# Performance work log

Measured on AMD Instinct MI355X. Metric: run time of the kernel, lower is better.

Reference implementation:

```python
import jax, jax.numpy as jnp
import numpy as np

B, D, DEPTH, C = 8192, 2048, 10, 1000
NUM_INNER = 2 ** DEPTH - 1   # 1023
NUM_LEAVES = 2 ** DEPTH      # 1024


def setup_inputs() -> dict:
    key = jax.random.key(0)
    k1, k2, k3, k4 = jax.random.split(key, 4)
    x = jax.random.normal(k1, (B, D), dtype=jnp.float32)
    # scale weights like a typical init so sigmoid isn't fully saturated
    W = jax.random.normal(k2, (D, NUM_INNER), dtype=jnp.float32) * 0.02
    b = jax.random.normal(k3, (NUM_INNER,), dtype=jnp.float32) * 0.02
    leaf_dist = jax.random.normal(k4, (NUM_LEAVES, C), dtype=jnp.float32)
    return {"x": x, "W": W, "b": b, "leaf_dist": leaf_dist}


def reference(x, W, b, leaf_dist):
    # inner node routing probabilities: [B, num_inner]
    decisions = jax.nn.sigmoid(x @ W + b)
    depth = int(np.log2(decisions.shape[1] + 1))
    pp = jnp.ones((x.shape[0], 1), dtype=x.dtype)  # path probs, starts at root
    for d in range(depth):  # small fixed loop over tree depth
        s, e = 2 ** d - 1, 2 ** (d + 1) - 1
        ld = decisions[:, s:e]                      # [B, 2^d]
        pp = jnp.concatenate([pp * ld, pp * (1.0 - ld)], axis=1)  # [B, 2^(d+1)]
        # faithful reproduction of the original's even/odd reordering
        pp = jnp.concatenate([pp[:, ::2], pp[:, 1::2]], axis=1)
    leaf_probs = jax.nn.softmax(leaf_dist, axis=1)  # [num_leaves, C]
    return pp @ leaf_probs                          # [B, C]
```

## Files before the change

kernel.cpp:

```cpp
#include <hip/hip_runtime.h>

typedef __attribute__((ext_vector_type(8))) unsigned short ushort8v;
typedef __attribute__((ext_vector_type(8))) __bf16 bf16x8;
typedef __attribute__((ext_vector_type(4))) float floatx4;

__device__ __forceinline__ unsigned short f2b(float f) {
    unsigned u = __float_as_uint(f);
    unsigned r = u + 0x7fffu + ((u >> 16) & 1u);
    return (unsigned short)(r >> 16);
}
__device__ __forceinline__ float b2f(unsigned short h) {
    return __uint_as_float(((unsigned)h) << 16);
}

__device__ __forceinline__ void async_cp16(const void* g, void* l) {
    __builtin_amdgcn_global_load_lds(
        (__attribute__((address_space(1))) void*)g,
        (__attribute__((address_space(3))) void*)l,
        16, 0, 0);
}

__global__ __launch_bounds__(256) void cvt_f32_bf16(const float* __restrict__ in,
                                                    unsigned short* __restrict__ out,
                                                    int n4) {
    int i = blockIdx.x * 256 + threadIdx.x;
    if (i < n4) {
        float4 v = ((const float4*)in)[i];
        ushort4 o;
        o.x = f2b(v.x); o.y = f2b(v.y); o.z = f2b(v.z); o.w = f2b(v.w);
        ((ushort4*)out)[i] = o;
    }
}

__global__ __launch_bounds__(256) void transpose_W(const float* __restrict__ W,
                                                   unsigned short* __restrict__ Wt) {
    __shared__ float tile[32][33];
    int tx = threadIdx.x, ty = threadIdx.y;
    int n0 = blockIdx.x * 32, k0 = blockIdx.y * 32;
#pragma unroll
    for (int i = 0; i < 4; i++) {
        int k = k0 + ty + i * 8, n = n0 + tx;
        tile[ty + i * 8][tx] = (n < 1023) ? W[(size_t)k * 1023 + n] : 0.f;
    }
    __syncthreads();
#pragma unroll
    for (int i = 0; i < 4; i++) {
        int n = n0 + ty + i * 8, k = k0 + tx;
        Wt[(size_t)n * 2048 + k] = f2b(tile[tx][ty + i * 8]);
    }
}

__global__ __launch_bounds__(256) void softmax_rows(const float* __restrict__ ld_,
                                                    unsigned short* __restrict__ P) {
    __shared__ float buf[1000];
    __shared__ float red[8];
    int t = threadIdx.x;
    const float* r = ld_ + (size_t)blockIdx.x * 1000;
    float mx = -3.4e38f;
    for (int i = t; i < 1000; i += 256) { float v = r[i]; buf[i] = v; mx = fmaxf(mx, v); }
#pragma unroll
    for (int o = 32; o > 0; o >>= 1) mx = fmaxf(mx, __shfl_down(mx, o));
    if ((t & 63) == 0) red[t >> 6] = mx;
    __syncthreads();
    mx = fmaxf(fmaxf(red[0], red[1]), fmaxf(red[2], red[3]));
    float s = 0.f;
    for (int i = t; i < 1000; i += 256) { float e = __expf(buf[i] - mx); buf[i] = e; s += e; }
#pragma unroll
    for (int o = 32; o > 0; o >>= 1) s += __shfl_down(s, o);
    if ((t & 63) == 0) red[4 + (t >> 6)] = s;
    __syncthreads();
    float inv = 1.f / (red[4] + red[5] + red[6] + red[7]);
    unsigned short* out = P + (size_t)blockIdx.x * 1000;
    for (int i = t; i < 1000; i += 256) out[i] = f2b(buf[i] * inv);
}

__global__ __launch_bounds__(256) void transpose_P(const unsigned short* __restrict__ P,
                                                   unsigned short* __restrict__ Pt) {
    __shared__ unsigned short tile[32][33];
    int tx = threadIdx.x, ty = threadIdx.y;
    int c0 = blockIdx.x * 32, l0 = blockIdx.y * 32;
#pragma unroll
    for (int i = 0; i < 4; i++) {
        int c = c0 + tx, l = l0 + ty + i * 8;
        tile[ty + i * 8][tx] = (c < 1000) ? P[(size_t)l * 1000 + c] : (unsigned short)0;
    }
    __syncthreads();
#pragma unroll
    for (int i = 0; i < 4; i++) {
        Pt[(size_t)(c0 + ty + i * 8) * 1024 + l0 + tx] = tile[tx][ty + i * 8];
    }
}

__global__ __launch_bounds__(256) void pp_kernel(unsigned short* __restrict__ dec) {
    __shared__ float d[1024];
    __shared__ float pa[1024], pb[1024];
    const int t = threadIdx.x;
    unsigned short* row = dec + (size_t)blockIdx.x * 1024;
    for (int i = t; i < 1024; i += 256) d[i] = (i < 1023) ? b2f(row[i]) : 0.f;
    if (t == 0) pa[0] = 1.f;
    __syncthreads();
    float* cur = pa; float* nxt = pb;
    for (int dep = 0; dep < 10; dep++) {
        const int half = 1 << dep;
        const int len = half << 1;
        for (int j = t; j < len; j += 256) {
            int tt = j >> dep;
            int s  = j & (half - 1);
            int i2 = 2 * s + tt;
            int u  = i2 >> dep;
            int rr = i2 & (half - 1);
            float dv = d[half - 1 + rr];
            nxt[j] = cur[rr] * (u ? (1.f - dv) : dv);
        }
        __syncthreads();
        float* tmp = cur; cur = nxt; nxt = tmp;
    }
    for (int i = t; i < 1024; i += 256) row[i] = f2b(cur[i]);
}

#define BM 128
#define BN 128
#define BK 32

template <int EPI>
__global__ __launch_bounds__(256) void gemm_bt(const unsigned short* __restrict__ A,
                                               const unsigned short* __restrict__ Bt,
                                               const float* __restrict__ bias,
                                               unsigned short* __restrict__ obf,
                                               float* __restrict__ of32,
                                               int K, int ldo) {
    __shared__ __align__(16) unsigned short As[BM * BK];
    __shared__ __align__(16) unsigned short Bs[BN * BK];
    const int tid  = threadIdx.x;
    const int lane = tid & 63;
    const int wave = tid >> 6;
    const int wr = wave >> 1, wc = wave & 1;
    const int quad = lane >> 4, l16 = lane & 15;

    const int l   = blockIdx.x;
    const int xcd = l & 7;
    const int j   = l >> 3;
    const int bm  = (xcd * 8 + (j & 7)) * BM;
    const int bn  = (j >> 3) * BN;

    const int srow = tid >> 2;
    const int lg   = (tid & 3) ^ ((srow >> 1) & 3);
    const int scol = lg * 8;

    const unsigned short* Ag = A + (size_t)(bm + srow) * K + scol;
    const unsigned short* Bg = Bt + (size_t)(bn + srow) * K + scol;
    unsigned short* AsW = As + wave * 512;
    unsigned short* BsW = Bs + wave * 512;

    const int pgA = (quad ^ ((l16 >> 1) & 3)) * 8;

    floatx4 acc[4][4] = {};

    for (int k0 = 0; k0 < K; k0 += BK) {
        async_cp16(Ag + k0, AsW);
        async_cp16(Ag + (size_t)64 * K + k0, AsW + 2048);
        async_cp16(Bg + k0, BsW);
        async_cp16(Bg + (size_t)64 * K + k0, BsW + 2048);
        __syncthreads();

        bf16x8 af[4], bfr[4];
#pragma unroll
        for (int mi = 0; mi < 4; mi++)
            af[mi] = __builtin_bit_cast(bf16x8,
                *(const ushort8v*)(As + (wr * 64 + mi * 16 + l16) * BK + pgA));
#pragma unroll
        for (int ni = 0; ni < 4; ni++)
            bfr[ni] = __builtin_bit_cast(bf16x8,
                *(const ushort8v*)(Bs + (wc * 64 + ni * 16 + l16) * BK + pgA));
#pragma unroll
        for (int mi = 0; mi < 4; mi++)
#pragma unroll
            for (int ni = 0; ni < 4; ni++)
                acc[mi][ni] = __builtin_amdgcn_mfma_f32_16x16x32_bf16(
                    af[mi], bfr[ni], acc[mi][ni], 0, 0, 0);
        __syncthreads();
    }

#pragma unroll
    for (int ni = 0; ni < 4; ni++) {
        const int col = bn + wc * 64 + ni * 16 + l16;
        float bb = 0.f;
        if constexpr (EPI == 0) bb = (col < 1023) ? bias[col] : 0.f;
#pragma unroll
        for (int mi = 0; mi < 4; mi++) {
            const int row0 = bm + wr * 64 + mi * 16 + quad * 4;
#pragma unroll
            for (int r = 0; r < 4; r++) {
                float v = acc[mi][ni][r];
                if constexpr (EPI == 0) {
                    float sgm = 1.f / (1.f + __expf(-(v + bb)));
                    obf[(size_t)(row0 + r) * ldo + col] = f2b(sgm);
                } else {
                    if (col < 1000) of32[(size_t)(row0 + r) * ldo + col] = v;
                }
            }
        }
    }
}

extern "C" void kernel_launch(void* const* d_in, const int* in_sizes, int n_in,
                              void* d_out, int out_size, void* d_ws, size_t ws_size,
                              hipStream_t stream) {
    const float* x   = (const float*)d_in[0];
    const float* W   = (const float*)d_in[1];
    const float* b   = (const float*)d_in[2];
    const float* ldd = (const float*)d_in[3];
    float* out = (float*)d_out;

    char* ws = (char*)d_ws;
    unsigned short* xb  = (unsigned short*)(ws);
    unsigned short* Wt  = (unsigned short*)(ws + 33554432);
    unsigned short* dec = (unsigned short*)(ws + 37748736);
    unsigned short* P   = (unsigned short*)(ws + 54525952);
    unsigned short* Pt  = (unsigned short*)(ws + 56574208);

    cvt_f32_bf16<<<16384, 256, 0, stream>>>(x, xb, 4194304);
    transpose_W<<<dim3(32, 64), dim3(32, 8), 0, stream>>>(W, Wt);
    softmax_rows<<<1024, 256, 0, stream>>>(ldd, P);
    transpose_P<<<dim3(32, 32), dim3(32, 8), 0, stream>>>(P, Pt);

    gemm_bt<0><<<512, 256, 0, stream>>>(xb, Wt, b, dec, nullptr, 2048, 1024);
    pp_kernel<<<8192, 256, 0, stream>>>(dec);
    gemm_bt<1><<<512, 256, 0, stream>>>(dec, Pt, nullptr, nullptr, out, 1024, 1000);
}
```

Before: 227.9 us.

## Merge prep kernels into combined launches and halve GEMM tile rows

Folds the x conversion, W transpose and leaf softmax into one launch, and the P transpose into the path-probability kernel, cutting seven launches to four. The GEMM tile shrinks from 128x128 to 64x128 with a doubled grid and a launch-bounds occupancy hint, which gives more blocks per CU on a 256-CU part. Smaller tiles lower operand reuse per block. The fused kernels' shared memory is sized for the largest branch, which can lower occupancy for the light blocks.

```diff
diff --git a/kernel.cpp b/kernel.cpp
--- a/kernel.cpp
+++ b/kernel.cpp
@@ -20,128 +20,130 @@
         16, 0, 0);
 }
 
-__global__ __launch_bounds__(256) void cvt_f32_bf16(const float* __restrict__ in,
-                                                    unsigned short* __restrict__ out,
-                                                    int n4) {
-    int i = blockIdx.x * 256 + threadIdx.x;
-    if (i < n4) {
-        float4 v = ((const float4*)in)[i];
+__global__ __launch_bounds__(256) void prep_kernel(const float* __restrict__ x,
+                                                   unsigned short* __restrict__ xb,
+                                                   const float* __restrict__ W,
+                                                   unsigned short* __restrict__ Wt,
+                                                   const float* __restrict__ ld_,
+                                                   unsigned short* __restrict__ P) {
+    __shared__ float tile[32 * 33];
+    __shared__ float buf[1000];
+    __shared__ float red[8];
+    const int b = blockIdx.x, t = threadIdx.x;
+    if (b < 16384) {
+        int i = b * 256 + t;
+        float4 v = ((const float4*)x)[i];
         ushort4 o;
         o.x = f2b(v.x); o.y = f2b(v.y); o.z = f2b(v.z); o.w = f2b(v.w);
-        ((ushort4*)out)[i] = o;
-    }
-}
-
-__global__ __launch_bounds__(256) void transpose_W(const float* __restrict__ W,
-                                                   unsigned short* __restrict__ Wt) {
-    __shared__ float tile[32][33];
-    int tx = threadIdx.x, ty = threadIdx.y;
-    int n0 = blockIdx.x * 32, k0 = blockIdx.y * 32;
-#pragma unroll
-    for (int i = 0; i < 4; i++) {
-        int k = k0 + ty + i * 8, n = n0 + tx;
-        tile[ty + i * 8][tx] = (n < 1023) ? W[(size_t)k * 1023 + n] : 0.f;
-    }
-    __syncthreads();
-#pragma unroll
-    for (int i = 0; i < 4; i++) {
-        int n = n0 + ty + i * 8, k = k0 + tx;
-        Wt[(size_t)n * 2048 + k] = f2b(tile[tx][ty + i * 8]);
-    }
-}
-
-__global__ __launch_bounds__(256) void softmax_rows(const float* __restrict__ ld_,
-                                                    unsigned short* __restrict__ P) {
-    __shared__ float buf[1000];
-    __shared__ float red[8];
-    int t = threadIdx.x;
-    const float* r = ld_ + (size_t)blockIdx.x * 1000;
-    float mx = -3.4e38f;
-    for (int i = t; i < 1000; i += 256) { float v = r[i]; buf[i] = v; mx = fmaxf(mx, v); }
-#pragma unroll
-    for (int o = 32; o > 0; o >>= 1) mx = fmaxf(mx, __shfl_down(mx, o));
-    if ((t & 63) == 0) red[t >> 6] = mx;
-    __syncthreads();
-    mx = fmaxf(fmaxf(red[0], red[1]), fmaxf(red[2], red[3]));
-    float s = 0.f;
-    for (int i = t; i < 1000; i += 256) { float e = __expf(buf[i] - mx); buf[i] = e; s += e; }
-#pragma unroll
-    for (int o = 32; o > 0; o >>= 1) s += __shfl_down(s, o);
-    if ((t & 63) == 0) red[4 + (t >> 6)] = s;
-    __syncthreads();
-    float inv = 1.f / (red[4] + red[5] + red[6] + red[7]);
-    unsigned short* out = P + (size_t)blockIdx.x * 1000;
-    for (int i = t; i < 1000; i += 256) out[i] = f2b(buf[i] * inv);
-}
-
-__global__ __launch_bounds__(256) void transpose_P(const unsigned short* __restrict__ P,
-                                                   unsigned short* __restrict__ Pt) {
-    __shared__ unsigned short tile[32][33];
-    int tx = threadIdx.x, ty = threadIdx.y;
-    int c0 = blockIdx.x * 32, l0 = blockIdx.y * 32;
-#pragma unroll
-    for (int i = 0; i < 4; i++) {
-        int c = c0 + tx, l = l0 + ty + i * 8;
-        tile[ty + i * 8][tx] = (c < 1000) ? P[(size_t)l * 1000 + c] : (unsigned short)0;
-    }
-    __syncthreads();
-#pragma unroll
-    for (int i = 0; i < 4; i++) {
-        Pt[(size_t)(c0 + ty + i * 8) * 1024 + l0 + tx] = tile[tx][ty + i * 8];
-    }
-}
-
-__global__ __launch_bounds__(256) void pp_kernel(unsigned short* __restrict__ dec) {
-    __shared__ float d[1024];
-    __shared__ float pa[1024], pb[1024];
-    const int t = threadIdx.x;
-    unsigned short* row = dec + (size_t)blockIdx.x * 1024;
-    for (int i = t; i < 1024; i += 256) d[i] = (i < 1023) ? b2f(row[i]) : 0.f;
-    if (t == 0) pa[0] = 1.f;
-    __syncthreads();
-    float* cur = pa; float* nxt = pb;
-    for (int dep = 0; dep < 10; dep++) {
-        const int half = 1 << dep;
-        const int len = half << 1;
-        for (int j = t; j < len; j += 256) {
-            int tt = j >> dep;
-            int s  = j & (half - 1);
-            int i2 = 2 * s + tt;
-            int u  = i2 >> dep;
-            int rr = i2 & (half - 1);
-            float dv = d[half - 1 + rr];
-            nxt[j] = cur[rr] * (u ? (1.f - dv) : dv);
-        }
-        __syncthreads();
-        float* tmp = cur; cur = nxt; nxt = tmp;
-    }
-    for (int i = t; i < 1024; i += 256) row[i] = f2b(cur[i]);
-}
-
-#define BM 128
+        ((ushort4*)xb)[i] = o;
+    } else if (b < 16384 + 2048) {
+        int idx = b - 16384;
+        int n0 = (idx & 31) * 32, k0 = (idx >> 5) * 32;
+        int tx = t & 31, ty = t >> 5;
+#pragma unroll
+        for (int i = 0; i < 4; i++) {
+            int k = k0 + ty + i * 8, n = n0 + tx;
+            tile[(ty + i * 8) * 33 + tx] = (n < 1023) ? W[(size_t)k * 1023 + n] : 0.f;
+        }
+        __syncthreads();
+#pragma unroll
+        for (int i = 0; i < 4; i++) {
+            int n = n0 + ty + i * 8, k = k0 + tx;
+            Wt[(size_t)n * 2048 + k] = f2b(tile[tx * 33 + ty + i * 8]);
+        }
+    } else {
+        int row = b - 18432;
+        const float* r = ld_ + (size_t)row * 1000;
+        float mx = -3.4e38f;
+        for (int i = t; i < 1000; i += 256) { float v = r[i]; buf[i] = v; mx = fmaxf(mx, v); }
+#pragma unroll
+        for (int o = 32; o > 0; o >>= 1) mx = fmaxf(mx, __shfl_down(mx, o));
+        if ((t & 63) == 0) red[t >> 6] = mx;
+        __syncthreads();
+        mx = fmaxf(fmaxf(red[0], red[1]), fmaxf(red[2], red[3]));
+        float s = 0.f;
+        for (int i = t; i < 1000; i += 256) { float e = __expf(buf[i] - mx); buf[i] = e; s += e; }
+#pragma unroll
+        for (int o = 32; o > 0; o >>= 1) s += __shfl_down(s, o);
+        if ((t & 63) == 0) red[4 + (t >> 6)] = s;
+        __syncthreads();
+        float inv = 1.f / (red[4] + red[5] + red[6] + red[7]);
+        unsigned short* out = P + (size_t)row * 1000;
+        for (int i = t; i < 1000; i += 256) out[i] = f2b(buf[i] * inv);
+    }
+}
+
+__global__ __launch_bounds__(256) void pp_transP_kernel(unsigned short* __restrict__ dec,
+                                                        const unsigned short* __restrict__ P,
+                                                        unsigned short* __restrict__ Pt) {
+    __shared__ float smem[3072];
+    const int b = blockIdx.x, t = threadIdx.x;
+    if (b < 8192) {
+        float* d = smem; float* pa = smem + 1024; float* pb = smem + 2048;
+        unsigned short* row = dec + (size_t)b * 1024;
+        for (int i = t; i < 1024; i += 256) d[i] = (i < 1023) ? b2f(row[i]) : 0.f;
+        if (t == 0) pa[0] = 1.f;
+        __syncthreads();
+        float* cur = pa; float* nxt = pb;
+        for (int dep = 0; dep < 10; dep++) {
+            const int half = 1 << dep;
+            const int len = half << 1;
+            for (int j = t; j < len; j += 256) {
+                int tt = j >> dep;
+                int s  = j & (half - 1);
+                int i2 = 2 * s + tt;
+                int u  = i2 >> dep;
+                int rr = i2 & (half - 1);
+                float dv = d[half - 1 + rr];
+                nxt[j] = cur[rr] * (u ? (1.f - dv) : dv);
+            }
+            __syncthreads();
+            float* tmp = cur; cur = nxt; nxt = tmp;
+        }
+        for (int i = t; i < 1024; i += 256) row[i] = f2b(cur[i]);
+    } else {
+        int idx = b - 8192;
+        int c0 = (idx & 31) * 32, l0 = (idx >> 5) * 32;
+        int tx = t & 31, ty = t >> 5;
+        unsigned short* tile = (unsigned short*)smem;
+#pragma unroll
+        for (int i = 0; i < 4; i++) {
+            int c = c0 + tx, l = l0 + ty + i * 8;
+            tile[(ty + i * 8) * 33 + tx] = (c < 1000) ? P[(size_t)l * 1000 + c] : (unsigned short)0;
+        }
+        __syncthreads();
+#pragma unroll
+        for (int i = 0; i < 4; i++) {
+            Pt[(size_t)(c0 + ty + i * 8) * 1024 + l0 + tx] = tile[tx * 33 + ty + i * 8];
+        }
+    }
+}
+
+#define BM 64
 #define BN 128
 #define BK 32
 
 template <int EPI>
-__global__ __launch_bounds__(256) void gemm_bt(const unsigned short* __restrict__ A,
-                                               const unsigned short* __restrict__ Bt,
-                                               const float* __restrict__ bias,
-                                               unsigned short* __restrict__ obf,
-                                               float* __restrict__ of32,
-                                               int K, int ldo) {
+__global__ __launch_bounds__(256, 4) void gemm_bt(const unsigned short* __restrict__ A,
+                                                  const unsigned short* __restrict__ Bt,
+                                                  const float* __restrict__ bias,
+                                                  unsigned short* __restrict__ obf,
+                                                  float* __restrict__ of32,
+                                                  int K, int ldo) {
     __shared__ __align__(16) unsigned short As[BM * BK];
     __shared__ __align__(16) unsigned short Bs[BN * BK];
     const int tid  = threadIdx.x;
     const int lane = tid & 63;
     const int wave = tid >> 6;
-    const int wr = wave >> 1, wc = wave & 1;
+    const int wrow = (wave >> 1) * 32;
+    const int wcol = (wave & 1) * 64;
     const int quad = lane >> 4, l16 = lane & 15;
 
     const int l   = blockIdx.x;
     const int xcd = l & 7;
     const int j   = l >> 3;
-    const int bm  = (xcd * 8 + (j & 7)) * BM;
-    const int bn  = (j >> 3) * BN;
+    const int bm  = (xcd * 16 + (j & 15)) * BM;
+    const int bn  = (j >> 4) * BN;
 
     const int srow = tid >> 2;
     const int lg   = (tid & 3) ^ ((srow >> 1) & 3);
@@ -152,28 +154,27 @@
     unsigned short* AsW = As + wave * 512;
     unsigned short* BsW = Bs + wave * 512;
 
-    const int pgA = (quad ^ ((l16 >> 1) & 3)) * 8;
-
-    floatx4 acc[4][4] = {};
+    const int pg = (quad ^ ((l16 >> 1) & 3)) * 8;
+
+    floatx4 acc[2][4] = {};
 
     for (int k0 = 0; k0 < K; k0 += BK) {
         async_cp16(Ag + k0, AsW);
-        async_cp16(Ag + (size_t)64 * K + k0, AsW + 2048);
         async_cp16(Bg + k0, BsW);
         async_cp16(Bg + (size_t)64 * K + k0, BsW + 2048);
         __syncthreads();
 
-        bf16x8 af[4], bfr[4];
-#pragma unroll
-        for (int mi = 0; mi < 4; mi++)
+        bf16x8 af[2], bfr[4];
+#pragma unroll
+        for (int mi = 0; mi < 2; mi++)
             af[mi] = __builtin_bit_cast(bf16x8,
-                *(const ushort8v*)(As + (wr * 64 + mi * 16 + l16) * BK + pgA));
+                *(const ushort8v*)(As + (wrow + mi * 16 + l16) * BK + pg));
 #pragma unroll
         for (int ni = 0; ni < 4; ni++)
             bfr[ni] = __builtin_bit_cast(bf16x8,
-                *(const ushort8v*)(Bs + (wc * 64 + ni * 16 + l16) * BK + pgA));
-#pragma unroll
-        for (int mi = 0; mi < 4; mi++)
+                *(const ushort8v*)(Bs + (wcol + ni * 16 + l16) * BK + pg));
+#pragma unroll
+        for (int mi = 0; mi < 2; mi++)
 #pragma unroll
             for (int ni = 0; ni < 4; ni++)
                 acc[mi][ni] = __builtin_amdgcn_mfma_f32_16x16x32_bf16(
@@ -183,12 +184,12 @@
 
 #pragma unroll
     for (int ni = 0; ni < 4; ni++) {
-        const int col = bn + wc * 64 + ni * 16 + l16;
+        const int col = bn + wcol + ni * 16 + l16;
         float bb = 0.f;
         if constexpr (EPI == 0) bb = (col < 1023) ? bias[col] : 0.f;
 #pragma unroll
-        for (int mi = 0; mi < 4; mi++) {
-            const int row0 = bm + wr * 64 + mi * 16 + quad * 4;
+        for (int mi = 0; mi < 2; mi++) {
+            const int row0 = bm + wrow + mi * 16 + quad * 4;
 #pragma unroll
             for (int r = 0; r < 4; r++) {
                 float v = acc[mi][ni][r];
@@ -219,12 +220,8 @@
     unsigned short* P   = (unsigned short*)(ws + 54525952);
     unsigned short* Pt  = (unsigned short*)(ws + 56574208);
 
-    cvt_f32_bf16<<<16384, 256, 0, stream>>>(x, xb, 4194304);
-    transpose_W<<<dim3(32, 64), dim3(32, 8), 0, stream>>>(W, Wt);
-    softmax_rows<<<1024, 256, 0, stream>>>(ldd, P);
-    transpose_P<<<dim3(32, 32), dim3(32, 8), 0, stream>>>(P, Pt);
-
-    gemm_bt<0><<<512, 256, 0, stream>>>(xb, Wt, b, dec, nullptr, 2048, 1024);
-    pp_kernel<<<8192, 256, 0, stream>>>(dec);
-    gemm_bt<1><<<512, 256, 0, stream>>>(dec, Pt, nullptr, nullptr, out, 1024, 1000);
-}
+    prep_kernel<<<16384 + 2048 + 1024, 256, 0, stream>>>(x, xb, W, Wt, ldd, P);
+    gemm_bt<0><<<1024, 256, 0, stream>>>(xb, Wt, b, dec, nullptr, 2048, 1024);
+    pp_transP_kernel<<<8192 + 1024, 256, 0, stream>>>(dec, P, Pt);
+    gemm_bt<1><<<1024, 256, 0, stream>>>(dec, Pt, nullptr, nullptr, out, 1024, 1000);
+}
```

Measured after the change: 219.4 us. 1.04x faster.
